# Optimization experiments

Hardware: AMD Instinct MI355X
Metric: run time of the kernel (lower is better)

Reference implementation:

```python
import jax, jax.numpy as jnp
import numpy as np

H = 2880
E = 8
K = 2
FF = 2880
CLIP = 7.0
AUX_COEF = 0.01
INIT_STD = 0.02
B, T = 2, 1024


def setup_inputs() -> dict:
    key = jax.random.key(0)
    ks = jax.random.split(key, 4)
    x = jax.random.normal(ks[0], (B, T, H), dtype=jnp.float32)
    W_in = INIT_STD * jax.random.normal(ks[1], (E, H, 2 * FF), dtype=jnp.float32)
    b_in = jnp.zeros((E, 2 * FF), dtype=jnp.float32)
    W_out = INIT_STD * jax.random.normal(ks[2], (E, FF, H), dtype=jnp.float32)
    b_out = jnp.zeros((E, H), dtype=jnp.float32)
    router_w = INIT_STD * jax.random.normal(ks[3], (E, H), dtype=jnp.float32)
    router_b = jnp.zeros((E,), dtype=jnp.float32)
    return {"x": x, "W_in": W_in, "b_in": b_in, "W_out": W_out,
            "b_out": b_out, "router_w": router_w, "router_b": router_b}


def reference(x, W_in, b_in, W_out, b_out, router_w, router_b):
    Bx, Tx, Hx = x.shape
    x_flat = x.reshape(-1, Hx)                       # [S, H]
    logits = x_flat @ router_w.T + router_b          # [S, E]

    topk_w, topk_idx = jax.lax.top_k(logits, K)      # [S, K]
    topk_w = jax.nn.softmax(topk_w.astype(jnp.float32), axis=-1).astype(x.dtype)
    one_hot = jax.nn.one_hot(topk_idx, E, dtype=x.dtype)        # [S, K, E]
    final_w = (one_hot * topk_w[..., None]).sum(axis=1)          # [S, E]

    probs = jax.nn.softmax(logits.astype(jnp.float32), axis=-1)  # [S, E]
    importance = probs.mean(axis=0)
    load = final_w.astype(jnp.float32).mean(axis=0)
    aux_loss = AUX_COEF * E * (importance * load).sum()

    # Dense over all experts (as in the original module)
    expert_in = jnp.einsum('sh,ehd->sed', x_flat, W_in) + b_in   # [S, E, 2FF]
    up, gate = jnp.split(expert_in, 2, axis=-1)
    up = jnp.clip(up, -CLIP, CLIP)
    gate = jnp.clip(gate, -CLIP, CLIP)
    act = jax.nn.silu(gate) * up                                 # [S, E, FF]
    expert_out = jnp.einsum('sef,efh->seh', act, W_out) + b_out  # [S, E, H]
    out = jnp.einsum('seh,se->sh', expert_out, final_w).reshape(Bx, Tx, Hx)

    expert_utilization = final_w.mean(axis=0)
    router_entropy = -(probs * jnp.log(probs + 1e-10)).sum(axis=-1).mean()
    return out, aux_loss, expert_utilization, router_entropy
```

## Files before the change

### kernel.cpp

```cpp
#include <hip/hip_runtime.h>
#include <hip/hip_bf16.h>
#include <cstdint>
#include <cstddef>

#define H_ 2880
#define E_ 8
#define FF_ 2880
#define TWO_FF 5760
#define S_ 2048
#define NPAD 5120
#define CLIPV 7.0f
#define AUXC 0.01f
#define NKB 45

#define GRID1 1280
#define GRID2 640

typedef __attribute__((ext_vector_type(8))) short bf16x8;
typedef __attribute__((ext_vector_type(4))) float f32x4;

#define WS_COUNTS   0
#define WS_FILL     32
#define WS_BASEP    64
#define WS_NS       104
#define WS_SCHED_E  128
#define WS_SCHED_C  5248
#define WS_SCHED_R  10368
#define WS_SCH2_E   15488
#define WS_SCH2_C   18048
#define WS_SCH2_R   20608
#define WS_IDX2     23168
#define WS_W2       39552
#define WS_PROBS    55936
#define WS_ENT      121472
#define WS_TOKL     129664
#define WS_ASSW     150144
#define WS_AG       262144
#define WS_TIN      29753344
#define WS_ACT      295174144
#define WS_TOUT     262144

typedef const __attribute__((address_space(1))) void global_cvoid;
typedef __attribute__((address_space(3))) void lds_void;

__device__ __forceinline__ void gload_lds16(const void* g, void* l) {
  __builtin_amdgcn_global_load_lds((global_cvoid*)g, (lds_void*)l, 16, 0, 0);
}

__device__ __forceinline__ unsigned int pack2bf(float a, float b) {
  __hip_bfloat162 h = __float22bfloat162_rn(make_float2(a, b));
  union { __hip_bfloat162 h; unsigned int u; } c; c.h = h; return c.u;
}

__device__ __forceinline__ unsigned short f2bf1(float f) {
  __hip_bfloat16 h = __float2bfloat16(f);
  union { __hip_bfloat16 h; unsigned short u; } c; c.h = h; return c.u;
}

__device__ __forceinline__ int xcd_lid(int bid, int ns) {
  int q = ns >> 3, r = ns & 7;
  int xcd = bid & 7, i = bid >> 3;
  int cnt = q + (xcd < r ? 1 : 0);
  if (i >= cnt) return -1;
  return xcd * q + (xcd < r ? xcd : r) + i;
}

__global__ void k_router(const float* __restrict__ x, const float* __restrict__ rw,
                         const float* __restrict__ rb, int* __restrict__ counts,
                         int* __restrict__ idx2, float* __restrict__ wtop,
                         float* __restrict__ probs, float* __restrict__ ent) {
  int wave = threadIdx.x >> 6, lane = threadIdx.x & 63;
  int s = blockIdx.x * 4 + wave;
  if (s >= S_) return;
  const float* xr = x + (size_t)s * H_;
  float acc[E_];
#pragma unroll
  for (int e = 0; e < E_; ++e) acc[e] = 0.f;
  for (int k = lane; k < H_; k += 64) {
    float xv = xr[k];
#pragma unroll
    for (int e = 0; e < E_; ++e) acc[e] = fmaf(xv, rw[e * H_ + k], acc[e]);
  }
#pragma unroll
  for (int e = 0; e < E_; ++e) {
#pragma unroll
    for (int off = 32; off > 0; off >>= 1) acc[e] += __shfl_xor(acc[e], off, 64);
    acc[e] += rb[e];
  }
  if (lane == 0) {
    int i1 = 0; float v1 = acc[0];
#pragma unroll
    for (int e = 1; e < E_; ++e) if (acc[e] > v1) { v1 = acc[e]; i1 = e; }
    int i2 = -1; float v2 = -3.4e38f;
#pragma unroll
    for (int e = 0; e < E_; ++e) if (e != i1 && acc[e] > v2) { v2 = acc[e]; i2 = e; }
    float w1 = 1.f / (1.f + expf(v2 - v1));
    float w2v = 1.f - w1;
    float m = v1;
    float se = 0.f; float p[E_];
#pragma unroll
    for (int e = 0; e < E_; ++e) { p[e] = expf(acc[e] - m); se += p[e]; }
    float inv = 1.f / se; float ents = 0.f;
#pragma unroll
    for (int e = 0; e < E_; ++e) {
      p[e] *= inv;
      ents -= p[e] * logf(p[e] + 1e-10f);
      probs[(size_t)s * E_ + e] = p[e];
    }
    ent[s] = ents;
    idx2[2 * s] = i1; idx2[2 * s + 1] = i2;
    wtop[2 * s] = w1; wtop[2 * s + 1] = w2v;
    atomicAdd(&counts[i1], 1); atomicAdd(&counts[i2], 1);
  }
}

__global__ void k_finalize(const int* __restrict__ counts, const float* __restrict__ probs,
                           const float* __restrict__ ent, const int* __restrict__ idx2,
                           const float* __restrict__ wtop, float* __restrict__ outsc,
                           int* __restrict__ basep, int* __restrict__ sched_e,
                           int* __restrict__ sched_c, int* __restrict__ sched_r,
                           int* __restrict__ s2e, int* __restrict__ s2c,
                           int* __restrict__ s2r, int* __restrict__ nsp) {
  __shared__ float red[256];
  __shared__ float tot[17];
  int t = threadIdx.x;
  float imp[8], ld[8]; float es = 0.f;
#pragma unroll
  for (int e = 0; e < 8; ++e) { imp[e] = 0.f; ld[e] = 0.f; }
  for (int s = t; s < S_; s += 256) {
#pragma unroll
    for (int e = 0; e < 8; ++e) imp[e] += probs[(size_t)s * 8 + e];
    es += ent[s];
    int e0 = idx2[2 * s], e1 = idx2[2 * s + 1];
    float a = wtop[2 * s], b = wtop[2 * s + 1];
#pragma unroll
    for (int e = 0; e < 8; ++e)
      ld[e] += (e0 == e ? a : 0.f) + (e1 == e ? b : 0.f);
  }
#pragma unroll
  for (int q = 0; q < 17; ++q) {
    float v = (q < 8) ? imp[q] : ((q < 16) ? ld[q - 8] : es);
    red[t] = v; __syncthreads();
    for (int o = 128; o > 0; o >>= 1) { if (t < o) red[t] += red[t + o]; __syncthreads(); }
    if (t == 0) tot[q] = red[0];
    __syncthreads();
  }
  if (t == 0) {
    float aux = 0.f;
#pragma unroll
    for (int e = 0; e < 8; ++e) aux += (tot[e] / (float)S_) * (tot[8 + e] / (float)S_);
    aux *= AUXC * (float)E_;
    outsc[0] = aux;
#pragma unroll
    for (int e = 0; e < 8; ++e) outsc[1 + e] = tot[8 + e] / (float)S_;
    outsc[9] = tot[16] / (float)S_;
    int bp = 0;
    for (int e = 0; e < 8; ++e) {
      basep[e] = bp;
      bp += ((counts[e] + 127) >> 7) << 7;
    }
    basep[8] = bp;
    int ns = 0;
    for (int e = 0; e < 8; ++e) {
      int tc = (counts[e] + 127) >> 7;
      for (int col = 0; col < 30; ++col)
        for (int tt = 0; tt < tc; ++tt) {
          sched_e[ns] = e; sched_c[ns] = col; sched_r[ns] = tt * 128; ++ns;
        }
    }
    nsp[0] = ns;
    int n2 = 0;
    for (int e = 0; e < 8; ++e) {
      int tc = (counts[e] + 127) >> 7;
      for (int col = 0; col < 15; ++col)
        for (int tt = 0; tt < tc; ++tt) {
          s2e[n2] = e; s2c[n2] = col; s2r[n2] = tt * 128; ++n2;
        }
    }
    nsp[1] = n2;
  }
}

__global__ void k_fill(const int* __restrict__ idx2, const float* __restrict__ wtop,
                       const int* __restrict__ basep, int* __restrict__ fill,
                       int* __restrict__ tokl, float* __restrict__ assw) {
  int s = blockIdx.x * 256 + threadIdx.x;
  if (s >= S_) return;
#pragma unroll
  for (int k = 0; k < 2; ++k) {
    int e = idx2[2 * s + k];
    int p = basep[e] + atomicAdd(&fill[e], 1);
    tokl[p] = s;
    assw[p] = wtop[2 * s + k];
  }
}

__global__ void k_gather(const float* __restrict__ x, const int* __restrict__ tokl,
                         unsigned short* __restrict__ Ag) {
  int g = blockIdx.x;
  int tok = tokl[g];
  int tm = g >> 7, r = g & 127;
  unsigned short* dst = Ag + (size_t)tm * 45 * 8192;
  const float* src = x + (size_t)tok * H_;
  for (int c = threadIdx.x; c < 360; c += 256) {
    float4 v0 = *(const float4*)(src + c * 8);
    float4 v1 = *(const float4*)(src + c * 8 + 4);
    uint4 o;
    o.x = pack2bf(v0.x, v0.y); o.y = pack2bf(v0.z, v0.w);
    o.z = pack2bf(v1.x, v1.y); o.w = pack2bf(v1.z, v1.w);
    *(uint4*)(dst + (size_t)(c >> 3) * 8192 + (c & 7) * 1024 + r * 8) = o;
  }
}

template <int LD>
__device__ __forceinline__ void convw_body(const float* __restrict__ src,
                                           unsigned short* __restrict__ dst,
                                           float (*ls)[97]) {
  int tid = threadIdx.x;
#pragma unroll
  for (int i = 0; i < 6; ++i) {
    int u = tid + 256 * i;
    int r = u / 24, c4 = u % 24;
    float4 v = *(const float4*)(src + (size_t)r * LD + c4 * 4);
    ls[r][c4 * 4 + 0] = v.x; ls[r][c4 * 4 + 1] = v.y;
    ls[r][c4 * 4 + 2] = v.z; ls[r][c4 * 4 + 3] = v.w;
  }
  __syncthreads();
#pragma unroll
  for (int i = 0; i < 3; ++i) {
    int ci = tid + 256 * i;
    int kq = ci / 96, n = ci % 96;
    float f[8];
#pragma unroll
    for (int j = 0; j < 8; ++j) f[j] = ls[kq * 8 + j][n];
    uint4 o;
    o.x = pack2bf(f[0], f[1]); o.y = pack2bf(f[2], f[3]);
    o.z = pack2bf(f[4], f[5]); o.w = pack2bf(f[6], f[7]);
    *(uint4*)(dst + ci * 8) = o;
  }
}

__global__ __launch_bounds__(256) void k_convw_in(const float* __restrict__ Win,
                                                  unsigned short* __restrict__ Tin) {
  __shared__ float ls[64][97];
  int bid = blockIdx.x;
  int e = bid / 2700, r = bid % 2700, nt = r / 45, kb = r % 45;
  const float* src = Win + (size_t)e * H_ * TWO_FF + (size_t)kb * 64 * TWO_FF + nt * 96;
  unsigned short* dst = Tin + (((size_t)e * 60 + nt) * 45 + kb) * 6144;
  convw_body<TWO_FF>(src, dst, ls);
}

__global__ __launch_bounds__(256) void k_convw_out(const float* __restrict__ Wout,
                                                   unsigned short* __restrict__ Tout) {
  __shared__ float ls[64][97];
  int bid = blockIdx.x;
  int e = bid / 1350, r = bid % 1350, nt = r / 45, kb = r % 45;
  const float* src = Wout + (size_t)e * FF_ * H_ + (size_t)kb * 64 * H_ + nt * 96;
  unsigned short* dst = Tout + (((size_t)e * 30 + nt) * 45 + kb) * 6144;
  convw_body<H_>(src, dst, ls);
}

__global__ __launch_bounds__(256, 2) void k_gemm1(
    const unsigned short* __restrict__ Ag, const unsigned short* __restrict__ Tin,
    const float* __restrict__ bin, const int* __restrict__ sched_e,
    const int* __restrict__ sched_c, const int* __restrict__ sched_r,
    const int* __restrict__ basep, const int* __restrict__ counts,
    const int* __restrict__ nsp, unsigned short* __restrict__ act) {
  __shared__ __align__(16) char lds[81920];
  int lid = xcd_lid(blockIdx.x, nsp[0]);
  if (lid < 0) return;
  int e = sched_e[lid], col = sched_c[lid], row0 = sched_r[lid];
  int n_e = counts[e], rbase = basep[e];
  int n0 = col * 96;
  int tid = threadIdx.x, lane = tid & 63, wv = tid >> 6;
  int wm = wv >> 1, wn = wv & 1;
  int tile_m = (rbase + row0) >> 7;

  const char* abase  = (const char*)Ag  + (size_t)tile_m * 45 * 16384;
  const char* bubase = (const char*)Tin + (((size_t)e * 60 + col) * 45) * 12288;
  const char* bgbase = (const char*)Tin + (((size_t)e * 60 + col + 30) * 45) * 12288;

#define ST1(BUF, KT) do {                                                        \
  const char* at_ = abase + (size_t)(KT) * 16384;                                \
  const char* bu_ = bubase + (size_t)(KT) * 12288;                               \
  const char* bg_ = bgbase + (size_t)(KT) * 12288;                               \
  _Pragma("unroll") for (int i_ = 0; i_ < 4; ++i_)                               \
    gload_lds16(at_ + (wv * 4 + i_) * 1024 + lane * 16,                          \
                lds + (BUF) * 16384 + (wv * 4 + i_) * 1024);                     \
  _Pragma("unroll") for (int i_ = 0; i_ < 3; ++i_) {                             \
    gload_lds16(bu_ + (wv * 3 + i_) * 1024 + lane * 16,                          \
                lds + 32768 + (BUF) * 12288 + (wv * 3 + i_) * 1024);             \
    gload_lds16(bg_ + (wv * 3 + i_) * 1024 + lane * 16,                          \
                lds + 57344 + (BUF) * 12288 + (wv * 3 + i_) * 1024); }           \
} while (0)

  f32x4 aU[4][3], aG[4][3];
#pragma unroll
  for (int m = 0; m < 4; ++m)
#pragma unroll
    for (int n = 0; n < 3; ++n) { aU[m][n] = (f32x4)0.f; aG[m][n] = (f32x4)0.f; }

  ST1(0, 0);
  int cur = 0;
  for (int kt = 0; kt < NKB; ++kt) {
    asm volatile("s_barrier" ::: "memory");
    if (kt + 1 < NKB) {
      ST1(cur ^ 1, kt + 1);
      asm volatile("s_waitcnt vmcnt(10)" ::: "memory");
    } else {
      asm volatile("s_waitcnt vmcnt(0)" ::: "memory");
    }
    asm volatile("s_barrier" ::: "memory");
    const char* Ab  = lds + cur * 16384 + (lane >> 4) * 2048 + (wm * 64 + (lane & 15)) * 16;
    const char* Bub = lds + 32768 + cur * 12288 + (lane >> 4) * 1536 + (wn * 48 + (lane & 15)) * 16;
    const char* Bgb = Bub + 24576;
#pragma unroll
    for (int s = 0; s < 2; ++s) {
      bf16x8 af[4], bu[3], bg[3];
#pragma unroll
      for (int m = 0; m < 4; ++m) af[m] = *(const bf16x8*)(Ab + s * 8192 + m * 256);
#pragma unroll
      for (int n = 0; n < 3; ++n) {
        bu[n] = *(const bf16x8*)(Bub + s * 6144 + n * 256);
        bg[n] = *(const bf16x8*)(Bgb + s * 6144 + n * 256);
      }
#pragma unroll
      for (int n = 0; n < 3; ++n)
#pragma unroll
        for (int m = 0; m < 4; ++m) {
          aU[m][n] = __builtin_amdgcn_mfma_f32_16x16x32_bf16(af[m], bu[n], aU[m][n], 0, 0, 0);
          aG[m][n] = __builtin_amdgcn_mfma_f32_16x16x32_bf16(af[m], bg[n], aG[m][n], 0, 0, 0);
        }
    }
    cur ^= 1;
  }
#undef ST1

  float bias_u[3], bias_g[3];
#pragma unroll
  for (int n = 0; n < 3; ++n) {
    int cidx = n0 + wn * 48 + n * 16 + (lane & 15);
    bias_u[n] = bin[(size_t)e * TWO_FF + cidx];
    bias_g[n] = bin[(size_t)e * TWO_FF + FF_ + cidx];
  }
  unsigned short* atile = act + (size_t)tile_m * 45 * 8192;
#pragma unroll
  for (int m = 0; m < 4; ++m) {
#pragma unroll
    for (int q = 0; q < 4; ++q) {
      int r = wm * 64 + m * 16 + (lane >> 4) * 4 + q;
      if (row0 + r < n_e) {
#pragma unroll
        for (int n = 0; n < 3; ++n) {
          int cidx = n0 + wn * 48 + n * 16 + (lane & 15);
          float u = aU[m][n][q] + bias_u[n];
          float g = aG[m][n][q] + bias_g[n];
          u = fminf(fmaxf(u, -CLIPV), CLIPV);
          g = fminf(fmaxf(g, -CLIPV), CLIPV);
          float sig = 1.f / (1.f + expf(-g));
          atile[(size_t)(cidx >> 6) * 8192 + ((cidx >> 3) & 7) * 1024 + r * 8 + (cidx & 7)]
              = f2bf1(g * sig * u);
        }
      }
    }
  }
}

__global__ __launch_bounds__(256, 2) void k_gemm2(
    const unsigned short* __restrict__ act, const unsigned short* __restrict__ Tout,
    const float* __restrict__ bout, const int* __restrict__ s2e,
    const int* __restrict__ s2c, const int* __restrict__ s2r,
    const int* __restrict__ basep, const int* __restrict__ counts,
    const int* __restrict__ nsp, const int* __restrict__ tokl,
    const float* __restrict__ assw, float* __restrict__ out) {
  __shared__ __align__(16) char lds[81920];
  int lid = xcd_lid(blockIdx.x, nsp[1]);
  if (lid < 0) return;
  int e = s2e[lid], col = s2c[lid], row0 = s2r[lid];
  int n_e = counts[e], rbase = basep[e];
  int n0 = col * 192;
  int tid = threadIdx.x, lane = tid & 63, wv = tid >> 6;
  int wm = wv >> 1, wn = wv & 1;
  int tile_m = (rbase + row0) >> 7;

  const char* abase = (const char*)act + (size_t)tile_m * 45 * 16384;
  const char* bbase = (const char*)Tout + (((size_t)e * 30 + col * 2) * 45) * 12288;

#define ST2(BUF, KT) do {                                                        \
  const char* at_ = abase + (size_t)(KT) * 16384;                                \
  _Pragma("unroll") for (int i_ = 0; i_ < 4; ++i_)                               \
    gload_lds16(at_ + (wv * 4 + i_) * 1024 + lane * 16,                          \
                lds + (BUF) * 16384 + (wv * 4 + i_) * 1024);                     \
  _Pragma("unroll") for (int i_ = 0; i_ < 6; ++i_) {                             \
    int ch_ = wv * 6 + i_;                                                       \
    const char* bt_ = bbase + (size_t)(ch_ / 12) * 45 * 12288                    \
                      + (size_t)(KT) * 12288 + (ch_ % 12) * 1024;                \
    gload_lds16(bt_ + lane * 16, lds + 32768 + (BUF) * 24576 + ch_ * 1024); }    \
} while (0)

  f32x4 acc[4][6];
#pragma unroll
  for (int m = 0; m < 4; ++m)
#pragma unroll
    for (int n = 0; n < 6; ++n) acc[m][n] = (f32x4)0.f;

  ST2(0, 0);
  int cur = 0;
  for (int kt = 0; kt < NKB; ++kt) {
    asm volatile("s_barrier" ::: "memory");
    if (kt + 1 < NKB) {
      ST2(cur ^ 1, kt + 1);
      asm volatile("s_waitcnt vmcnt(10)" ::: "memory");
    } else {
      asm volatile("s_waitcnt vmcnt(0)" ::: "memory");
    }
    asm volatile("s_barrier" ::: "memory");
    const char* Ab = lds + cur * 16384 + (lane >> 4) * 2048 + (wm * 64 + (lane & 15)) * 16;
    const char* Bb = lds + 32768 + cur * 24576 + wn * 12288 + (lane >> 4) * 1536 + (lane & 15) * 16;
#pragma unroll
    for (int s = 0; s < 2; ++s) {
      bf16x8 af[4], bf[6];
#pragma unroll
      for (int m = 0; m < 4; ++m) af[m] = *(const bf16x8*)(Ab + s * 8192 + m * 256);
#pragma unroll
      for (int n = 0; n < 6; ++n) bf[n] = *(const bf16x8*)(Bb + s * 6144 + n * 256);
#pragma unroll
      for (int n = 0; n < 6; ++n)
#pragma unroll
        for (int m = 0; m < 4; ++m)
          acc[m][n] = __builtin_amdgcn_mfma_f32_16x16x32_bf16(af[m], bf[n], acc[m][n], 0, 0, 0);
    }
    cur ^= 1;
  }
#undef ST2

  float bb[6];
#pragma unroll
  for (int n = 0; n < 6; ++n)
    bb[n] = bout[(size_t)e * H_ + n0 + wn * 96 + n * 16 + (lane & 15)];
#pragma unroll
  for (int m = 0; m < 4; ++m) {
#pragma unroll
    for (int q = 0; q < 4; ++q) {
      int r = wm * 64 + m * 16 + (lane >> 4) * 4 + q;
      if (row0 + r < n_e) {
        int g = rbase + row0 + r;
        int tok = tokl[g];
        float w = assw[g];
        float* orow = out + (size_t)tok * H_;
#pragma unroll
        for (int n = 0; n < 6; ++n) {
          int cidx = n0 + wn * 96 + n * 16 + (lane & 15);
          atomicAdd(&orow[cidx], w * (acc[m][n][q] + bb[n]));
        }
      }
    }
  }
}

extern "C" void kernel_launch(void* const* d_in, const int* in_sizes, int n_in,
                              void* d_out, int out_size, void* d_ws, size_t ws_size,
                              hipStream_t stream) {
  (void)in_sizes; (void)n_in; (void)ws_size;
  const float* x        = (const float*)d_in[0];
  const float* W_in     = (const float*)d_in[1];
  const float* b_in     = (const float*)d_in[2];
  const float* W_out    = (const float*)d_in[3];
  const float* b_out    = (const float*)d_in[4];
  const float* router_w = (const float*)d_in[5];
  const float* router_b = (const float*)d_in[6];
  float* out = (float*)d_out;
  char* ws = (char*)d_ws;

  int*   counts  = (int*)(ws + WS_COUNTS);
  int*   fill    = (int*)(ws + WS_FILL);
  int*   basep   = (int*)(ws + WS_BASEP);
  int*   nsp     = (int*)(ws + WS_NS);
  int*   sched_e = (int*)(ws + WS_SCHED_E);
  int*   sched_c = (int*)(ws + WS_SCHED_C);
  int*   sched_r = (int*)(ws + WS_SCHED_R);
  int*   s2e     = (int*)(ws + WS_SCH2_E);
  int*   s2c     = (int*)(ws + WS_SCH2_C);
  int*   s2r     = (int*)(ws + WS_SCH2_R);
  int*   idx2    = (int*)(ws + WS_IDX2);
  float* wtop    = (float*)(ws + WS_W2);
  float* probs   = (float*)(ws + WS_PROBS);
  float* ent     = (float*)(ws + WS_ENT);
  int*   tokl    = (int*)(ws + WS_TOKL);
  float* assw    = (float*)(ws + WS_ASSW);
  unsigned short* Ag   = (unsigned short*)(ws + WS_AG);
  unsigned short* Tin  = (unsigned short*)(ws + WS_TIN);
  unsigned short* actp = (unsigned short*)(ws + WS_ACT);
  unsigned short* Tout = (unsigned short*)(ws + WS_TOUT);

  hipMemsetAsync(ws + WS_COUNTS, 0, 128, stream);
  hipMemsetAsync(ws + WS_TOKL, 0, NPAD * 4, stream);
  hipMemsetAsync(d_out, 0, (size_t)out_size * sizeof(float), stream);

  k_router<<<S_ / 4, 256, 0, stream>>>(x, router_w, router_b, counts, idx2, wtop, probs, ent);
  k_finalize<<<1, 256, 0, stream>>>(counts, probs, ent, idx2, wtop,
                                    out + (size_t)S_ * H_, basep, sched_e, sched_c, sched_r,
                                    s2e, s2c, s2r, nsp);
  k_fill<<<S_ / 256, 256, 0, stream>>>(idx2, wtop, basep, fill, tokl, assw);
  k_gather<<<NPAD, 256, 0, stream>>>(x, tokl, Ag);
  k_convw_in<<<21600, 256, 0, stream>>>(W_in, Tin);
  k_gemm1<<<GRID1, 256, 0, stream>>>(Ag, Tin, b_in, sched_e, sched_c, sched_r,
                                     basep, counts, nsp, actp);
  k_convw_out<<<10800, 256, 0, stream>>>(W_out, Tout);
  k_gemm2<<<GRID2, 256, 0, stream>>>(actp, Tout, b_out, s2e, s2c, s2r,
                                     basep, counts, nsp, tokl, assw, out);
}
```

Measured before the change: 707.2 us.

## Co-schedule weight conversion with router and GEMM1 to overlap bandwidth work

The W_in bf16 conversion moves into one launch with the router, and the W_out conversion runs inside the GEMM1 launch on 3 of every 4 block slots. The gather/fill step folds into finalize, which now builds the schedules in parallel and uses LDS atomics. The aim is to overlap memory-bound conversion with compute-bound GEMM and to cut launch count and serial single-thread scheduling. Tout gets its own workspace region because it can no longer alias Ag while GEMM1 runs. This risks imbalance if conversion blocks finish much later than the GEMM blocks, and GEMM1 block ids become less XCD-aware.

```diff
diff --git a/kernel.cpp b/kernel.cpp
--- a/kernel.cpp
+++ b/kernel.cpp
@@ -13,14 +13,14 @@
 #define AUXC 0.01f
 #define NKB 45
 
-#define GRID1 1280
-#define GRID2 640
+#define GRIDP  22112
+#define GRID1C 5120
+#define GRID2  640
 
 typedef __attribute__((ext_vector_type(8))) short bf16x8;
 typedef __attribute__((ext_vector_type(4))) float f32x4;
 
 #define WS_COUNTS   0
-#define WS_FILL     32
 #define WS_BASEP    64
 #define WS_NS       104
 #define WS_SCHED_E  128
@@ -38,7 +38,7 @@
 #define WS_AG       262144
 #define WS_TIN      29753344
 #define WS_ACT      295174144
-#define WS_TOUT     262144
+#define WS_TOUT     324665344
 
 typedef const __attribute__((address_space(1))) void global_cvoid;
 typedef __attribute__((address_space(3))) void lds_void;
@@ -65,12 +65,52 @@
   return xcd * q + (xcd < r ? xcd : r) + i;
 }
 
-__global__ void k_router(const float* __restrict__ x, const float* __restrict__ rw,
-                         const float* __restrict__ rb, int* __restrict__ counts,
-                         int* __restrict__ idx2, float* __restrict__ wtop,
-                         float* __restrict__ probs, float* __restrict__ ent) {
+template <int LD>
+__device__ __forceinline__ void convw_body(const float* __restrict__ src,
+                                           unsigned short* __restrict__ dst,
+                                           float (*ls)[97]) {
+  int tid = threadIdx.x;
+#pragma unroll
+  for (int i = 0; i < 6; ++i) {
+    int u = tid + 256 * i;
+    int r = u / 24, c4 = u % 24;
+    float4 v = *(const float4*)(src + (size_t)r * LD + c4 * 4);
+    ls[r][c4 * 4 + 0] = v.x; ls[r][c4 * 4 + 1] = v.y;
+    ls[r][c4 * 4 + 2] = v.z; ls[r][c4 * 4 + 3] = v.w;
+  }
+  __syncthreads();
+#pragma unroll
+  for (int i = 0; i < 3; ++i) {
+    int ci = tid + 256 * i;
+    int kq = ci / 96, n = ci % 96;
+    float f[8];
+#pragma unroll
+    for (int j = 0; j < 8; ++j) f[j] = ls[kq * 8 + j][n];
+    uint4 o;
+    o.x = pack2bf(f[0], f[1]); o.y = pack2bf(f[2], f[3]);
+    o.z = pack2bf(f[4], f[5]); o.w = pack2bf(f[6], f[7]);
+    *(uint4*)(dst + ci * 8) = o;
+  }
+}
+
+__global__ __launch_bounds__(256) void k_pre(
+    const float* __restrict__ Win, unsigned short* __restrict__ Tin,
+    const float* __restrict__ x, const float* __restrict__ rw,
+    const float* __restrict__ rb, int* __restrict__ counts,
+    int* __restrict__ idx2, float* __restrict__ wtop,
+    float* __restrict__ probs, float* __restrict__ ent) {
+  __shared__ float ls[64][97];
+  int bid = blockIdx.x;
+  if (bid < 21600) {
+    int e = bid / 2700, r = bid % 2700, nt = r / 45, kb = r % 45;
+    const float* src = Win + (size_t)e * H_ * TWO_FF + (size_t)kb * 64 * TWO_FF + nt * 96;
+    unsigned short* dst = Tin + (((size_t)e * 60 + nt) * 45 + kb) * 6144;
+    convw_body<TWO_FF>(src, dst, ls);
+    return;
+  }
+  int rbid = bid - 21600;
   int wave = threadIdx.x >> 6, lane = threadIdx.x & 63;
-  int s = blockIdx.x * 4 + wave;
+  int s = rbid * 4 + wave;
   if (s >= S_) return;
   const float* xr = x + (size_t)s * H_;
   float acc[E_];
@@ -120,9 +160,11 @@
                            int* __restrict__ basep, int* __restrict__ sched_e,
                            int* __restrict__ sched_c, int* __restrict__ sched_r,
                            int* __restrict__ s2e, int* __restrict__ s2c,
-                           int* __restrict__ s2r, int* __restrict__ nsp) {
+                           int* __restrict__ s2r, int* __restrict__ nsp,
+                           int* __restrict__ tokl, float* __restrict__ assw) {
   __shared__ float red[256];
   __shared__ float tot[17];
+  __shared__ int sh_tc[8], sh_cum[9], sh_base[9], sfill[8];
   int t = threadIdx.x;
   float imp[8], ld[8]; float es = 0.f;
 #pragma unroll
@@ -154,44 +196,45 @@
 #pragma unroll
     for (int e = 0; e < 8; ++e) outsc[1 + e] = tot[8 + e] / (float)S_;
     outsc[9] = tot[16] / (float)S_;
-    int bp = 0;
-    for (int e = 0; e < 8; ++e) {
-      basep[e] = bp;
-      bp += ((counts[e] + 127) >> 7) << 7;
-    }
-    basep[8] = bp;
-    int ns = 0;
+    int bp = 0, cum = 0;
     for (int e = 0; e < 8; ++e) {
       int tc = (counts[e] + 127) >> 7;
-      for (int col = 0; col < 30; ++col)
-        for (int tt = 0; tt < tc; ++tt) {
-          sched_e[ns] = e; sched_c[ns] = col; sched_r[ns] = tt * 128; ++ns;
-        }
-    }
-    nsp[0] = ns;
-    int n2 = 0;
-    for (int e = 0; e < 8; ++e) {
-      int tc = (counts[e] + 127) >> 7;
-      for (int col = 0; col < 15; ++col)
-        for (int tt = 0; tt < tc; ++tt) {
-          s2e[n2] = e; s2c[n2] = col; s2r[n2] = tt * 128; ++n2;
-        }
-    }
-    nsp[1] = n2;
-  }
-}
-
-__global__ void k_fill(const int* __restrict__ idx2, const float* __restrict__ wtop,
-                       const int* __restrict__ basep, int* __restrict__ fill,
-                       int* __restrict__ tokl, float* __restrict__ assw) {
-  int s = blockIdx.x * 256 + threadIdx.x;
-  if (s >= S_) return;
-#pragma unroll
-  for (int k = 0; k < 2; ++k) {
-    int e = idx2[2 * s + k];
-    int p = basep[e] + atomicAdd(&fill[e], 1);
-    tokl[p] = s;
-    assw[p] = wtop[2 * s + k];
+      sh_tc[e] = tc; sh_cum[e] = cum; sh_base[e] = bp;
+      basep[e] = bp;
+      cum += tc; bp += tc << 7;
+    }
+    sh_cum[8] = cum; sh_base[8] = bp; basep[8] = bp;
+    nsp[0] = cum * 30; nsp[1] = cum * 15;
+  }
+  if (t < 8) sfill[t] = 0;
+  __syncthreads();
+  int ntile = sh_cum[8];
+  int ns1 = ntile * 30;
+  for (int sidx = t; sidx < ns1; sidx += 256) {
+    int e = 0;
+    while (e < 7 && sidx >= sh_cum[e + 1] * 30) ++e;
+    int tc = sh_tc[e];
+    int rem = sidx - sh_cum[e] * 30;
+    int col = rem / tc, tt = rem - col * tc;
+    sched_e[sidx] = e; sched_c[sidx] = col; sched_r[sidx] = tt * 128;
+  }
+  int ns2 = ntile * 15;
+  for (int sidx = t; sidx < ns2; sidx += 256) {
+    int e = 0;
+    while (e < 7 && sidx >= sh_cum[e + 1] * 15) ++e;
+    int tc = sh_tc[e];
+    int rem = sidx - sh_cum[e] * 15;
+    int col = rem / tc, tt = rem - col * tc;
+    s2e[sidx] = e; s2c[sidx] = col; s2r[sidx] = tt * 128;
+  }
+  for (int s = t; s < S_; s += 256) {
+#pragma unroll
+    for (int k = 0; k < 2; ++k) {
+      int e = idx2[2 * s + k];
+      int p = sh_base[e] + atomicAdd(&sfill[e], 1);
+      tokl[p] = s;
+      assw[p] = wtop[2 * s + k];
+    }
   }
 }
 
@@ -212,63 +255,31 @@
   }
 }
 
-template <int LD>
-__device__ __forceinline__ void convw_body(const float* __restrict__ src,
-                                           unsigned short* __restrict__ dst,
-                                           float (*ls)[97]) {
-  int tid = threadIdx.x;
-#pragma unroll
-  for (int i = 0; i < 6; ++i) {
-    int u = tid + 256 * i;
-    int r = u / 24, c4 = u % 24;
-    float4 v = *(const float4*)(src + (size_t)r * LD + c4 * 4);
-    ls[r][c4 * 4 + 0] = v.x; ls[r][c4 * 4 + 1] = v.y;
-    ls[r][c4 * 4 + 2] = v.z; ls[r][c4 * 4 + 3] = v.w;
-  }
-  __syncthreads();
-#pragma unroll
-  for (int i = 0; i < 3; ++i) {
-    int ci = tid + 256 * i;
-    int kq = ci / 96, n = ci % 96;
-    float f[8];
-#pragma unroll
-    for (int j = 0; j < 8; ++j) f[j] = ls[kq * 8 + j][n];
-    uint4 o;
-    o.x = pack2bf(f[0], f[1]); o.y = pack2bf(f[2], f[3]);
-    o.z = pack2bf(f[4], f[5]); o.w = pack2bf(f[6], f[7]);
-    *(uint4*)(dst + ci * 8) = o;
-  }
-}
-
-__global__ __launch_bounds__(256) void k_convw_in(const float* __restrict__ Win,
-                                                  unsigned short* __restrict__ Tin) {
-  __shared__ float ls[64][97];
-  int bid = blockIdx.x;
-  int e = bid / 2700, r = bid % 2700, nt = r / 45, kb = r % 45;
-  const float* src = Win + (size_t)e * H_ * TWO_FF + (size_t)kb * 64 * TWO_FF + nt * 96;
-  unsigned short* dst = Tin + (((size_t)e * 60 + nt) * 45 + kb) * 6144;
-  convw_body<TWO_FF>(src, dst, ls);
-}
-
-__global__ __launch_bounds__(256) void k_convw_out(const float* __restrict__ Wout,
-                                                   unsigned short* __restrict__ Tout) {
-  __shared__ float ls[64][97];
-  int bid = blockIdx.x;
-  int e = bid / 1350, r = bid % 1350, nt = r / 45, kb = r % 45;
-  const float* src = Wout + (size_t)e * FF_ * H_ + (size_t)kb * 64 * H_ + nt * 96;
-  unsigned short* dst = Tout + (((size_t)e * 30 + nt) * 45 + kb) * 6144;
-  convw_body<H_>(src, dst, ls);
-}
-
-__global__ __launch_bounds__(256, 2) void k_gemm1(
+__global__ __launch_bounds__(256, 2) void k_gemm1c(
     const unsigned short* __restrict__ Ag, const unsigned short* __restrict__ Tin,
     const float* __restrict__ bin, const int* __restrict__ sched_e,
     const int* __restrict__ sched_c, const int* __restrict__ sched_r,
     const int* __restrict__ basep, const int* __restrict__ counts,
-    const int* __restrict__ nsp, unsigned short* __restrict__ act) {
+    const int* __restrict__ nsp, unsigned short* __restrict__ act,
+    const float* __restrict__ Wout, unsigned short* __restrict__ Tout) {
   __shared__ __align__(16) char lds[81920];
-  int lid = xcd_lid(blockIdx.x, nsp[0]);
-  if (lid < 0) return;
+  int bid = blockIdx.x;
+  int g = bid >> 5, p = bid & 31, phase = g & 3;
+  if ((p & 3) != phase) {
+    int nless = (p >> 2) + (((p & 3) > phase) ? 1 : 0);
+    int cid = g * 24 + (p - nless);
+    float (*ls)[97] = (float(*)[97])lds;
+    for (int tile = cid; tile < 10800; tile += 3840) {
+      int e = tile / 1350, r2 = tile % 1350, nt = r2 / 45, kb = r2 % 45;
+      const float* src = Wout + (size_t)e * FF_ * H_ + (size_t)kb * 64 * H_ + nt * 96;
+      unsigned short* dst = Tout + (((size_t)e * 30 + nt) * 45 + kb) * 6144;
+      convw_body<H_>(src, dst, ls);
+      __syncthreads();
+    }
+    return;
+  }
+  int lid = g * 8 + (p >> 2);
+  if (lid >= nsp[0]) return;
   int e = sched_e[lid], col = sched_c[lid], row0 = sched_r[lid];
   int n_e = counts[e], rbase = basep[e];
   int n0 = col * 96;
@@ -354,12 +365,12 @@
         for (int n = 0; n < 3; ++n) {
           int cidx = n0 + wn * 48 + n * 16 + (lane & 15);
           float u = aU[m][n][q] + bias_u[n];
-          float g = aG[m][n][q] + bias_g[n];
+          float gg = aG[m][n][q] + bias_g[n];
           u = fminf(fmaxf(u, -CLIPV), CLIPV);
-          g = fminf(fmaxf(g, -CLIPV), CLIPV);
-          float sig = 1.f / (1.f + expf(-g));
+          gg = fminf(fmaxf(gg, -CLIPV), CLIPV);
+          float sig = 1.f / (1.f + expf(-gg));
           atile[(size_t)(cidx >> 6) * 8192 + ((cidx >> 3) & 7) * 1024 + r * 8 + (cidx & 7)]
-              = f2bf1(g * sig * u);
+              = f2bf1(gg * sig * u);
         }
       }
     }
@@ -473,7 +484,6 @@
   char* ws = (char*)d_ws;
 
   int*   counts  = (int*)(ws + WS_COUNTS);
-  int*   fill    = (int*)(ws + WS_FILL);
   int*   basep   = (int*)(ws + WS_BASEP);
   int*   nsp     = (int*)(ws + WS_NS);
   int*   sched_e = (int*)(ws + WS_SCHED_E);
@@ -497,16 +507,15 @@
   hipMemsetAsync(ws + WS_TOKL, 0, NPAD * 4, stream);
   hipMemsetAsync(d_out, 0, (size_t)out_size * sizeof(float), stream);
 
-  k_router<<<S_ / 4, 256, 0, stream>>>(x, router_w, router_b, counts, idx2, wtop, probs, ent);
+  k_pre<<<GRIDP, 256, 0, stream>>>(W_in, Tin, x, router_w, router_b,
+                                   counts, idx2, wtop, probs, ent);
   k_finalize<<<1, 256, 0, stream>>>(counts, probs, ent, idx2, wtop,
-                                    out + (size_t)S_ * H_, basep, sched_e, sched_c, sched_r,
-                                    s2e, s2c, s2r, nsp);
-  k_fill<<<S_ / 256, 256, 0, stream>>>(idx2, wtop, basep, fill, tokl, assw);
+                                    out + (size_t)S_ * H_, basep,
+                                    sched_e, sched_c, sched_r,
+                                    s2e, s2c, s2r, nsp, tokl, assw);
   k_gather<<<NPAD, 256, 0, stream>>>(x, tokl, Ag);
-  k_convw_in<<<21600, 256, 0, stream>>>(W_in, Tin);
-  k_gemm1<<<GRID1, 256, 0, stream>>>(Ag, Tin, b_in, sched_e, sched_c, sched_r,
-                                     basep, counts, nsp, actp);
-  k_convw_out<<<10800, 256, 0, stream>>>(W_out, Tout);
+  k_gemm1c<<<GRID1C, 256, 0, stream>>>(Ag, Tin, b_in, sched_e, sched_c, sched_r,
+                                       basep, counts, nsp, actp, W_out, Tout);
   k_gemm2<<<GRID2, 256, 0, stream>>>(actp, Tout, b_out, s2e, s2c, s2r,
                                      basep, counts, nsp, tokl, assw, out);
 }
```

After: 647.9 us. -8.4%, faster.
